# Optimization experiments

Measured on AMD Instinct MI355X. Metric: run time of the kernel, lower is better.

Reference implementation:

```python
import jax, jax.numpy as jnp
import numpy as np

N_NODES = 100000
N_EDGES = 1600000
D_IN = 64
D_OUT = 64


def setup_inputs() -> dict:
    key = jax.random.key(0)
    k1, k2, k3, k4, k5, k6 = jax.random.split(key, 6)
    x = jax.random.normal(k1, (N_NODES, D_IN), dtype=jnp.float32)
    edge_index = jax.random.randint(k2, (2, N_EDGES), 0, N_NODES, dtype=jnp.int64)
    edge_weight = jax.random.uniform(k3, (N_EDGES,), dtype=jnp.float32)
    scale = 1.0 / np.sqrt(D_IN)
    W0 = jax.random.normal(k4, (D_IN, D_OUT), dtype=jnp.float32) * scale
    W1 = jax.random.normal(k5, (D_IN, D_OUT), dtype=jnp.float32) * scale
    b = jax.random.normal(k6, (D_OUT,), dtype=jnp.float32) * 0.01
    return {"x": x, "edge_index": edge_index, "edge_weight": edge_weight,
            "W0": W0, "W1": W1, "b": b}


def reference(x, edge_index, edge_weight, W0, W1, b):
    # ChebConv K=2 with default lambda_max=2.0, sym normalization:
    # L_hat = 2L/lambda_max - I = -D^{-1/2} A D^{-1/2}
    N = x.shape[0]
    row, col = edge_index[0], edge_index[1]
    deg = jax.ops.segment_sum(edge_weight, row, num_segments=N)  # [N]
    deg_safe = jnp.where(deg > 0, deg, 1.0)
    dinv = jnp.where(deg > 0, jax.lax.rsqrt(deg_safe), 0.0)
    norm = -dinv[row] * edge_weight * dinv[col]  # [E], L_hat edge weights
    # Tx_1[i] = sum_{e: col_e = i} norm_e * x[row_e]
    Tx1 = jax.ops.segment_sum(norm[:, None] * x[row], col, num_segments=N)
    # out = lin0(Tx_0) + lin1(Tx_1) + bias
    return x @ W0 + Tx1 @ W1 + b
```

## Files before the change

### kernel.cpp

```cpp
#include <hip/hip_runtime.h>

#define N_NODES 100000
#define N_EDGES 1600000
#define D 64
#define NB 256
#define EPB (N_EDGES / NB)
#define NBUCK 3125
#define CAP 1024
#define ST 68

__global__ __launch_bounds__(256) void count_kernel(const int* __restrict__ row,
                                                    const int* __restrict__ col,
                                                    int* __restrict__ matC,
                                                    int* __restrict__ matR) {
    __shared__ int cC[NBUCK];
    __shared__ int cR[NBUCK];
    int t = threadIdx.x;
    for (int j = t; j < NBUCK; j += 256) { cC[j] = 0; cR[j] = 0; }
    __syncthreads();
    int base = blockIdx.x * EPB;
    for (int i = t; i < EPB; i += 256) {
        int e = base + i;
        atomicAdd(&cC[col[e] >> 5], 1);
        atomicAdd(&cR[row[e] >> 5], 1);
    }
    __syncthreads();
    int* mc = matC + (size_t)blockIdx.x * NBUCK;
    int* mr = matR + (size_t)blockIdx.x * NBUCK;
    for (int j = t; j < NBUCK; j += 256) { mc[j] = cC[j]; mr[j] = cR[j]; }
}

__global__ __launch_bounds__(NB) void blockscan_kernel(int* __restrict__ matC,
                                                       int* __restrict__ matR,
                                                       int* __restrict__ totalsC,
                                                       int* __restrict__ totalsR) {
    int which  = blockIdx.x / NBUCK;
    int bucket = blockIdx.x % NBUCK;
    int* mat    = which ? matR : matC;
    int* totals = which ? totalsR : totalsC;
    __shared__ int lds[NB];
    int t = threadIdx.x;
    int v = mat[(size_t)t * NBUCK + bucket];
    lds[t] = v;
    __syncthreads();
    for (int off = 1; off < NB; off <<= 1) {
        int u = (t >= off) ? lds[t - off] : 0;
        __syncthreads();
        lds[t] += u;
        __syncthreads();
    }
    mat[(size_t)t * NBUCK + bucket] = (t > 0) ? lds[t - 1] : 0;
    if (t == NB - 1) totals[bucket] = lds[NB - 1];
}

__global__ __launch_bounds__(256) void totscan_kernel(const int* __restrict__ totalsC,
                                                      int* __restrict__ bstartC,
                                                      const int* __restrict__ totalsR,
                                                      int* __restrict__ bstartR) {
    const int* tot = blockIdx.x ? totalsR : totalsC;
    int* bst       = blockIdx.x ? bstartR : bstartC;
    const int CH = (NBUCK + 255) / 256;
    __shared__ int lds[256];
    int t = threadIdx.x;
    int local[CH];
    int s = 0;
    for (int i = 0; i < CH; ++i) {
        int idx = t * CH + i;
        local[i] = (idx < NBUCK) ? tot[idx] : 0;
        s += local[i];
    }
    lds[t] = s;
    __syncthreads();
    for (int off = 1; off < 256; off <<= 1) {
        int u = (t >= off) ? lds[t - off] : 0;
        __syncthreads();
        lds[t] += u;
        __syncthreads();
    }
    int excl = (t > 0) ? lds[t - 1] : 0;
    for (int i = 0; i < CH; ++i) {
        int idx = t * CH + i;
        if (idx < NBUCK) bst[idx] = excl;
        excl += local[i];
    }
}

__global__ __launch_bounds__(256) void scatter_kernel(const int* __restrict__ row,
                                                      const int* __restrict__ col,
                                                      const float* __restrict__ w,
                                                      const int* __restrict__ matC,
                                                      const int* __restrict__ matR,
                                                      const int* __restrict__ bstartC,
                                                      const int* __restrict__ bstartR,
                                                      int2* __restrict__ crecs,
                                                      unsigned* __restrict__ rrecs) {
    __shared__ int cursC[NBUCK];
    __shared__ int cursR[NBUCK];
    int t = threadIdx.x;
    const int* offC = matC + (size_t)blockIdx.x * NBUCK;
    const int* offR = matR + (size_t)blockIdx.x * NBUCK;
    for (int j = t; j < NBUCK; j += 256) {
        cursC[j] = bstartC[j] + offC[j];
        cursR[j] = bstartR[j] + offR[j];
    }
    __syncthreads();
    int base = blockIdx.x * EPB;
    for (int i = t; i < EPB; i += 256) {
        int e = base + i;
        int r = row[e];
        int c = col[e];
        float we = w[e];
        int pC = atomicAdd(&cursC[c >> 5], 1);
        crecs[pC] = make_int2(r | ((c & 31) << 17), __float_as_int(we));
        int pR = atomicAdd(&cursR[r >> 5], 1);
        rrecs[pR] = (__float_as_uint(we) & ~31u) | (unsigned)(r & 31);
    }
}

__global__ __launch_bounds__(256) void deg_kernel(const unsigned* __restrict__ rrecs,
                                                  const int* __restrict__ bstartR,
                                                  const int* __restrict__ totalsR,
                                                  float* __restrict__ dinv) {
    __shared__ float acc[32];
    int t = threadIdx.x;
    int b = blockIdx.x;
    if (t < 32) acc[t] = 0.f;
    __syncthreads();
    int base = bstartR[b];
    int cnt  = totalsR[b];
    for (int i = t; i < cnt; i += 256) {
        unsigned v = rrecs[base + i];
        atomicAdd(&acc[v & 31u], __uint_as_float(v & ~31u));
    }
    __syncthreads();
    if (t < 32) {
        float d = acc[t];
        dinv[b * 32 + t] = d > 0.f ? rsqrtf(d) : 0.f;
    }
}

__global__ __launch_bounds__(256) void gather_out_kernel(
        const int2* __restrict__ crecs, const int* __restrict__ bstartC,
        const int* __restrict__ totalsC, const float* __restrict__ dinv,
        const float* __restrict__ x,
        const float* __restrict__ W0, const float* __restrict__ W1,
        const float* __restrict__ bias, float* __restrict__ out) {
    __shared__ __align__(16) char smem[32 * ST * 4 * 2];
    int2* raw = (int2*)smem;
    int2* srt = (int2*)(smem + 8192);
    int*  cnt32   = (int*)(smem + 16384);
    int*  start32 = cnt32 + 32;
    int*  cur32   = cnt32 + 64;
    float* xs = (float*)smem;
    float* ts = (float*)(smem + 32 * ST * 4);

    int tid = threadIdx.x;
    int b   = blockIdx.x;
    int n0  = b * 32;
    int n   = tid >> 3;
    int j   = tid & 7;

    int base = bstartC[b];
    int cnt  = totalsC[b];

    float4 acc0 = make_float4(0.f, 0.f, 0.f, 0.f);
    float4 acc1 = make_float4(0.f, 0.f, 0.f, 0.f);
    const float* xj = x + (size_t)(j << 3);

    for (int cb = 0; cb < cnt; cb += CAP) {
        int m = min(CAP, cnt - cb);
        if (tid < 32) cnt32[tid] = 0;
        __syncthreads();
        for (int i = tid; i < m; i += 256) {
            int2 rec = crecs[base + cb + i];
            raw[i] = rec;
            atomicAdd(&cnt32[((unsigned)rec.x) >> 17], 1);
        }
        __syncthreads();
        if (tid == 0) {
            int s = 0;
            for (int k = 0; k < 32; ++k) {
                int v = cnt32[k]; start32[k] = s; cur32[k] = s; s += v;
            }
        }
        __syncthreads();
        for (int i = tid; i < m; i += 256) {
            int2 rec = raw[i];
            int p = atomicAdd(&cur32[((unsigned)rec.x) >> 17], 1);
            srt[p] = rec;
        }
        __syncthreads();
        int ks = start32[n];
        int ke = ks + cnt32[n];
        int k = ks;
        for (; k + 1 < ke; k += 2) {
            int2 ra = srt[k];
            int2 rb = srt[k + 1];
            int r0 = ra.x & 0x1FFFF;
            int r1 = rb.x & 0x1FFFF;
            float c0 = __int_as_float(ra.y) * dinv[r0];
            float c1 = __int_as_float(rb.y) * dinv[r1];
            const float* p0 = xj + (size_t)r0 * D;
            const float* p1 = xj + (size_t)r1 * D;
            float4 a0 = *(const float4*)p0;
            float4 a1 = *(const float4*)(p0 + 4);
            float4 b0 = *(const float4*)p1;
            float4 b1 = *(const float4*)(p1 + 4);
            acc0.x += c0 * a0.x; acc0.y += c0 * a0.y; acc0.z += c0 * a0.z; acc0.w += c0 * a0.w;
            acc1.x += c0 * a1.x; acc1.y += c0 * a1.y; acc1.z += c0 * a1.z; acc1.w += c0 * a1.w;
            acc0.x += c1 * b0.x; acc0.y += c1 * b0.y; acc0.z += c1 * b0.z; acc0.w += c1 * b0.w;
            acc1.x += c1 * b1.x; acc1.y += c1 * b1.y; acc1.z += c1 * b1.z; acc1.w += c1 * b1.w;
        }
        if (k < ke) {
            int2 ra = srt[k];
            int r0 = ra.x & 0x1FFFF;
            float c0 = __int_as_float(ra.y) * dinv[r0];
            const float* p0 = xj + (size_t)r0 * D;
            float4 a0 = *(const float4*)p0;
            float4 a1 = *(const float4*)(p0 + 4);
            acc0.x += c0 * a0.x; acc0.y += c0 * a0.y; acc0.z += c0 * a0.z; acc0.w += c0 * a0.w;
            acc1.x += c0 * a1.x; acc1.y += c0 * a1.y; acc1.z += c0 * a1.z; acc1.w += c0 * a1.w;
        }
        __syncthreads();
    }

    float dn = -dinv[n0 + n];
    float* tp = ts + n * ST + (j << 3);
    *(float4*)tp       = make_float4(dn * acc0.x, dn * acc0.y, dn * acc0.z, dn * acc0.w);
    *(float4*)(tp + 4) = make_float4(dn * acc1.x, dn * acc1.y, dn * acc1.z, dn * acc1.w);
    for (int i = tid; i < 512; i += 256) {
        int nn = i >> 4;
        int kk = (i & 15) << 2;
        *(float4*)&xs[nn * ST + kk] = *(const float4*)(x + (size_t)n0 * D + i * 4);
    }
    __syncthreads();

    int jl = j << 3;
    float4 o0 = *(const float4*)(bias + jl);
    float4 o1 = *(const float4*)(bias + jl + 4);
    for (int k = 0; k < D; k += 4) {
        float4 av = *(const float4*)&xs[n * ST + k];
        float4 tv = *(const float4*)&ts[n * ST + k];
        #pragma unroll
        for (int u = 0; u < 4; ++u) {
            float a = (u == 0) ? av.x : (u == 1) ? av.y : (u == 2) ? av.z : av.w;
            float t = (u == 0) ? tv.x : (u == 1) ? tv.y : (u == 2) ? tv.z : tv.w;
            const float4 w00 = *(const float4*)(W0 + (size_t)(k + u) * D + jl);
            const float4 w01 = *(const float4*)(W0 + (size_t)(k + u) * D + jl + 4);
            const float4 w10 = *(const float4*)(W1 + (size_t)(k + u) * D + jl);
            const float4 w11 = *(const float4*)(W1 + (size_t)(k + u) * D + jl + 4);
            o0.x += a * w00.x + t * w10.x;
            o0.y += a * w00.y + t * w10.y;
            o0.z += a * w00.z + t * w10.z;
            o0.w += a * w00.w + t * w10.w;
            o1.x += a * w01.x + t * w11.x;
            o1.y += a * w01.y + t * w11.y;
            o1.z += a * w01.z + t * w11.z;
            o1.w += a * w01.w + t * w11.w;
        }
    }
    float* op = out + (size_t)(n0 + n) * D + jl;
    *(float4*)op       = o0;
    *(float4*)(op + 4) = o1;
}

extern "C" void kernel_launch(void* const* d_in, const int* in_sizes, int n_in,
                              void* d_out, int out_size, void* d_ws, size_t ws_size,
                              hipStream_t stream) {
    const float* x    = (const float*)d_in[0];
    const int*   eidx = (const int*)d_in[1];
    const float* ew   = (const float*)d_in[2];
    const float* W0   = (const float*)d_in[3];
    const float* W1   = (const float*)d_in[4];
    const float* b    = (const float*)d_in[5];
    float* out = (float*)d_out;

    const int* row = eidx;
    const int* col = eidx + N_EDGES;

    int2*     crecs   = (int2*)d_ws;
    unsigned* rrecs   = (unsigned*)((int*)d_ws + 2 * (size_t)N_EDGES);
    int*      matC    = (int*)rrecs + N_EDGES;
    int*      matR    = matC + (size_t)NB * NBUCK;
    int*      totalsC = matR + (size_t)NB * NBUCK;
    int*      bstartC = totalsC + NBUCK;
    int*      totalsR = bstartC + NBUCK;
    int*      bstartR = totalsR + NBUCK;
    float*    dinv    = (float*)(bstartR + NBUCK);

    count_kernel     <<<NB, 256, 0, stream>>>(row, col, matC, matR);
    blockscan_kernel <<<2 * NBUCK, NB, 0, stream>>>(matC, matR, totalsC, totalsR);
    totscan_kernel   <<<2, 256, 0, stream>>>(totalsC, bstartC, totalsR, bstartR);
    scatter_kernel   <<<NB, 256, 0, stream>>>(row, col, ew, matC, matR,
                                              bstartC, bstartR, crecs, rrecs);
    deg_kernel       <<<NBUCK, 256, 0, stream>>>(rrecs, bstartR, totalsR, dinv);
    gather_out_kernel<<<NBUCK, 256, 0, stream>>>(crecs, bstartC, totalsC, dinv,
                                                 x, W0, W1, b, out);
}
```

Baseline: 337.0 us.

## Tile the bucket-offset scan, halve partition blocks, and unroll the gather loop

```diff
diff --git a/kernel.cpp b/kernel.cpp
--- a/kernel.cpp
+++ b/kernel.cpp
@@ -3,54 +3,91 @@
 #define N_NODES 100000
 #define N_EDGES 1600000
 #define D 64
-#define NB 256
+#define NB 128
 #define EPB (N_EDGES / NB)
 #define NBUCK 3125
+#define NBUCK_PAD 3136
+#define NGRP 98
 #define CAP 1024
 #define ST 68
 
-__global__ __launch_bounds__(256) void count_kernel(const int* __restrict__ row,
+__global__ __launch_bounds__(512) void count_kernel(const int* __restrict__ row,
                                                     const int* __restrict__ col,
                                                     int* __restrict__ matC,
                                                     int* __restrict__ matR) {
-    __shared__ int cC[NBUCK];
-    __shared__ int cR[NBUCK];
-    int t = threadIdx.x;
-    for (int j = t; j < NBUCK; j += 256) { cC[j] = 0; cR[j] = 0; }
+    __shared__ int cC[NBUCK_PAD];
+    __shared__ int cR[NBUCK_PAD];
+    int t = threadIdx.x;
+    for (int j = t; j < NBUCK_PAD; j += 512) { cC[j] = 0; cR[j] = 0; }
     __syncthreads();
     int base = blockIdx.x * EPB;
-    for (int i = t; i < EPB; i += 256) {
+    for (int i = t; i < EPB; i += 512) {
         int e = base + i;
         atomicAdd(&cC[col[e] >> 5], 1);
         atomicAdd(&cR[row[e] >> 5], 1);
     }
     __syncthreads();
-    int* mc = matC + (size_t)blockIdx.x * NBUCK;
-    int* mr = matR + (size_t)blockIdx.x * NBUCK;
-    for (int j = t; j < NBUCK; j += 256) { mc[j] = cC[j]; mr[j] = cR[j]; }
-}
-
-__global__ __launch_bounds__(NB) void blockscan_kernel(int* __restrict__ matC,
-                                                       int* __restrict__ matR,
-                                                       int* __restrict__ totalsC,
-                                                       int* __restrict__ totalsR) {
-    int which  = blockIdx.x / NBUCK;
-    int bucket = blockIdx.x % NBUCK;
+    int* mc = matC + (size_t)blockIdx.x * NBUCK_PAD;
+    int* mr = matR + (size_t)blockIdx.x * NBUCK_PAD;
+    for (int j = t; j < NBUCK_PAD; j += 512) { mc[j] = cC[j]; mr[j] = cR[j]; }
+}
+
+__global__ __launch_bounds__(256) void blockscan_kernel(int* __restrict__ matC,
+                                                        int* __restrict__ matR,
+                                                        int* __restrict__ totalsC,
+                                                        int* __restrict__ totalsR) {
+    int which = blockIdx.x / NGRP;
+    int grp   = blockIdx.x % NGRP;
     int* mat    = which ? matR : matC;
     int* totals = which ? totalsR : totalsC;
-    __shared__ int lds[NB];
-    int t = threadIdx.x;
-    int v = mat[(size_t)t * NBUCK + bucket];
-    lds[t] = v;
-    __syncthreads();
-    for (int off = 1; off < NB; off <<= 1) {
-        int u = (t >= off) ? lds[t - off] : 0;
-        __syncthreads();
-        lds[t] += u;
-        __syncthreads();
-    }
-    mat[(size_t)t * NBUCK + bucket] = (t > 0) ? lds[t - 1] : 0;
-    if (t == NB - 1) totals[bucket] = lds[NB - 1];
+    int j0 = grp * 32;
+    __shared__ int tile[NB][33];
+    int t = threadIdx.x;
+    int r = t >> 1;
+    int h = t & 1;
+    {
+        const int* src = mat + (size_t)r * NBUCK_PAD + j0 + h * 16;
+        int4 v0 = *(const int4*)(src + 0);
+        int4 v1 = *(const int4*)(src + 4);
+        int4 v2 = *(const int4*)(src + 8);
+        int4 v3 = *(const int4*)(src + 12);
+        int cb = h * 16;
+        tile[r][cb+0]=v0.x;  tile[r][cb+1]=v0.y;  tile[r][cb+2]=v0.z;  tile[r][cb+3]=v0.w;
+        tile[r][cb+4]=v1.x;  tile[r][cb+5]=v1.y;  tile[r][cb+6]=v1.z;  tile[r][cb+7]=v1.w;
+        tile[r][cb+8]=v2.x;  tile[r][cb+9]=v2.y;  tile[r][cb+10]=v2.z; tile[r][cb+11]=v2.w;
+        tile[r][cb+12]=v3.x; tile[r][cb+13]=v3.y; tile[r][cb+14]=v3.z; tile[r][cb+15]=v3.w;
+    }
+    __syncthreads();
+    int g = t >> 3;
+    int l = t & 7;
+    int rows0 = l * 16;
+    int vals[16];
+    int s = 0;
+    #pragma unroll
+    for (int i = 0; i < 16; ++i) { vals[i] = tile[rows0 + i][g]; s += vals[i]; }
+    int inc = s;
+    #pragma unroll
+    for (int d = 1; d < 8; d <<= 1) {
+        int u = __shfl_up(inc, d, 8);
+        if (l >= d) inc += u;
+    }
+    int excl = inc - s;
+    #pragma unroll
+    for (int i = 0; i < 16; ++i) { int e2 = excl; excl += vals[i]; tile[rows0 + i][g] = e2; }
+    if (l == 7) totals[j0 + g] = inc;
+    __syncthreads();
+    {
+        int* dst = mat + (size_t)r * NBUCK_PAD + j0 + h * 16;
+        int cb = h * 16;
+        int4 v0 = make_int4(tile[r][cb+0],  tile[r][cb+1],  tile[r][cb+2],  tile[r][cb+3]);
+        int4 v1 = make_int4(tile[r][cb+4],  tile[r][cb+5],  tile[r][cb+6],  tile[r][cb+7]);
+        int4 v2 = make_int4(tile[r][cb+8],  tile[r][cb+9],  tile[r][cb+10], tile[r][cb+11]);
+        int4 v3 = make_int4(tile[r][cb+12], tile[r][cb+13], tile[r][cb+14], tile[r][cb+15]);
+        *(int4*)(dst + 0)  = v0;
+        *(int4*)(dst + 4)  = v1;
+        *(int4*)(dst + 8)  = v2;
+        *(int4*)(dst + 12) = v3;
+    }
 }
 
 __global__ __launch_bounds__(256) void totscan_kernel(const int* __restrict__ totalsC,
@@ -59,14 +96,14 @@
                                                       int* __restrict__ bstartR) {
     const int* tot = blockIdx.x ? totalsR : totalsC;
     int* bst       = blockIdx.x ? bstartR : bstartC;
-    const int CH = (NBUCK + 255) / 256;
+    const int CH = (NBUCK_PAD + 255) / 256;
     __shared__ int lds[256];
     int t = threadIdx.x;
     int local[CH];
     int s = 0;
     for (int i = 0; i < CH; ++i) {
         int idx = t * CH + i;
-        local[i] = (idx < NBUCK) ? tot[idx] : 0;
+        local[i] = (idx < NBUCK_PAD) ? tot[idx] : 0;
         s += local[i];
     }
     lds[t] = s;
@@ -80,12 +117,12 @@
     int excl = (t > 0) ? lds[t - 1] : 0;
     for (int i = 0; i < CH; ++i) {
         int idx = t * CH + i;
-        if (idx < NBUCK) bst[idx] = excl;
+        if (idx < NBUCK_PAD) bst[idx] = excl;
         excl += local[i];
     }
 }
 
-__global__ __launch_bounds__(256) void scatter_kernel(const int* __restrict__ row,
+__global__ __launch_bounds__(512) void scatter_kernel(const int* __restrict__ row,
                                                       const int* __restrict__ col,
                                                       const float* __restrict__ w,
                                                       const int* __restrict__ matC,
@@ -97,15 +134,15 @@
     __shared__ int cursC[NBUCK];
     __shared__ int cursR[NBUCK];
     int t = threadIdx.x;
-    const int* offC = matC + (size_t)blockIdx.x * NBUCK;
-    const int* offR = matR + (size_t)blockIdx.x * NBUCK;
-    for (int j = t; j < NBUCK; j += 256) {
+    const int* offC = matC + (size_t)blockIdx.x * NBUCK_PAD;
+    const int* offR = matR + (size_t)blockIdx.x * NBUCK_PAD;
+    for (int j = t; j < NBUCK; j += 512) {
         cursC[j] = bstartC[j] + offC[j];
         cursR[j] = bstartR[j] + offR[j];
     }
     __syncthreads();
     int base = blockIdx.x * EPB;
-    for (int i = t; i < EPB; i += 256) {
+    for (int i = t; i < EPB; i += 512) {
         int e = base + i;
         int r = row[e];
         int c = col[e];
@@ -138,6 +175,10 @@
         dinv[b * 32 + t] = d > 0.f ? rsqrtf(d) : 0.f;
     }
 }
+
+#define FMA8(cc, av, bv)                                                       \
+    acc0.x += cc * av.x; acc0.y += cc * av.y; acc0.z += cc * av.z; acc0.w += cc * av.w; \
+    acc1.x += cc * bv.x; acc1.y += cc * bv.y; acc1.z += cc * bv.z; acc1.w += cc * bv.w;
 
 __global__ __launch_bounds__(256) void gather_out_kernel(
         const int2* __restrict__ crecs, const int* __restrict__ bstartC,
@@ -173,15 +214,22 @@
         __syncthreads();
         for (int i = tid; i < m; i += 256) {
             int2 rec = crecs[base + cb + i];
+            int r = rec.x & 0x1FFFF;
+            rec.y = __float_as_int(__int_as_float(rec.y) * dinv[r]);
             raw[i] = rec;
             atomicAdd(&cnt32[((unsigned)rec.x) >> 17], 1);
         }
         __syncthreads();
-        if (tid == 0) {
-            int s = 0;
-            for (int k = 0; k < 32; ++k) {
-                int v = cnt32[k]; start32[k] = s; cur32[k] = s; s += v;
+        if (tid < 32) {
+            int v = cnt32[tid];
+            int inc = v;
+            #pragma unroll
+            for (int d = 1; d < 32; d <<= 1) {
+                int u = __shfl_up(inc, d, 32);
+                if (tid >= d) inc += u;
             }
+            start32[tid] = inc - v;
+            cur32[tid]   = inc - v;
         }
         __syncthreads();
         for (int i = tid; i < m; i += 256) {
@@ -193,33 +241,34 @@
         int ks = start32[n];
         int ke = ks + cnt32[n];
         int k = ks;
-        for (; k + 1 < ke; k += 2) {
-            int2 ra = srt[k];
-            int2 rb = srt[k + 1];
-            int r0 = ra.x & 0x1FFFF;
-            int r1 = rb.x & 0x1FFFF;
-            float c0 = __int_as_float(ra.y) * dinv[r0];
-            float c1 = __int_as_float(rb.y) * dinv[r1];
-            const float* p0 = xj + (size_t)r0 * D;
-            const float* p1 = xj + (size_t)r1 * D;
-            float4 a0 = *(const float4*)p0;
-            float4 a1 = *(const float4*)(p0 + 4);
-            float4 b0 = *(const float4*)p1;
-            float4 b1 = *(const float4*)(p1 + 4);
-            acc0.x += c0 * a0.x; acc0.y += c0 * a0.y; acc0.z += c0 * a0.z; acc0.w += c0 * a0.w;
-            acc1.x += c0 * a1.x; acc1.y += c0 * a1.y; acc1.z += c0 * a1.z; acc1.w += c0 * a1.w;
-            acc0.x += c1 * b0.x; acc0.y += c1 * b0.y; acc0.z += c1 * b0.z; acc0.w += c1 * b0.w;
-            acc1.x += c1 * b1.x; acc1.y += c1 * b1.y; acc1.z += c1 * b1.z; acc1.w += c1 * b1.w;
-        }
-        if (k < ke) {
-            int2 ra = srt[k];
-            int r0 = ra.x & 0x1FFFF;
-            float c0 = __int_as_float(ra.y) * dinv[r0];
-            const float* p0 = xj + (size_t)r0 * D;
-            float4 a0 = *(const float4*)p0;
-            float4 a1 = *(const float4*)(p0 + 4);
-            acc0.x += c0 * a0.x; acc0.y += c0 * a0.y; acc0.z += c0 * a0.z; acc0.w += c0 * a0.w;
-            acc1.x += c0 * a1.x; acc1.y += c0 * a1.y; acc1.z += c0 * a1.z; acc1.w += c0 * a1.w;
+        for (; k + 3 < ke; k += 4) {
+            int2 e0 = srt[k + 0];
+            int2 e1 = srt[k + 1];
+            int2 e2 = srt[k + 2];
+            int2 e3 = srt[k + 3];
+            const float* p0 = xj + (size_t)(e0.x & 0x1FFFF) * D;
+            const float* p1 = xj + (size_t)(e1.x & 0x1FFFF) * D;
+            const float* p2 = xj + (size_t)(e2.x & 0x1FFFF) * D;
+            const float* p3 = xj + (size_t)(e3.x & 0x1FFFF) * D;
+            float c0 = __int_as_float(e0.y);
+            float c1 = __int_as_float(e1.y);
+            float c2 = __int_as_float(e2.y);
+            float c3 = __int_as_float(e3.y);
+            float4 a0 = *(const float4*)p0, b0 = *(const float4*)(p0 + 4);
+            float4 a1 = *(const float4*)p1, b1 = *(const float4*)(p1 + 4);
+            float4 a2 = *(const float4*)p2, b2 = *(const float4*)(p2 + 4);
+            float4 a3 = *(const float4*)p3, b3 = *(const float4*)(p3 + 4);
+            FMA8(c0, a0, b0)
+            FMA8(c1, a1, b1)
+            FMA8(c2, a2, b2)
+            FMA8(c3, a3, b3)
+        }
+        for (; k < ke; ++k) {
+            int2 e0 = srt[k];
+            const float* p0 = xj + (size_t)(e0.x & 0x1FFFF) * D;
+            float c0 = __int_as_float(e0.y);
+            float4 a0 = *(const float4*)p0, b0 = *(const float4*)(p0 + 4);
+            FMA8(c0, a0, b0)
         }
         __syncthreads();
     }
@@ -281,17 +330,17 @@
     int2*     crecs   = (int2*)d_ws;
     unsigned* rrecs   = (unsigned*)((int*)d_ws + 2 * (size_t)N_EDGES);
     int*      matC    = (int*)rrecs + N_EDGES;
-    int*      matR    = matC + (size_t)NB * NBUCK;
-    int*      totalsC = matR + (size_t)NB * NBUCK;
-    int*      bstartC = totalsC + NBUCK;
-    int*      totalsR = bstartC + NBUCK;
-    int*      bstartR = totalsR + NBUCK;
-    float*    dinv    = (float*)(bstartR + NBUCK);
-
-    count_kernel     <<<NB, 256, 0, stream>>>(row, col, matC, matR);
-    blockscan_kernel <<<2 * NBUCK, NB, 0, stream>>>(matC, matR, totalsC, totalsR);
+    int*      matR    = matC + (size_t)NB * NBUCK_PAD;
+    int*      totalsC = matR + (size_t)NB * NBUCK_PAD;
+    int*      bstartC = totalsC + NBUCK_PAD;
+    int*      totalsR = bstartC + NBUCK_PAD;
+    int*      bstartR = totalsR + NBUCK_PAD;
+    float*    dinv    = (float*)(bstartR + NBUCK_PAD);
+
+    count_kernel     <<<NB, 512, 0, stream>>>(row, col, matC, matR);
+    blockscan_kernel <<<2 * NGRP, 256, 0, stream>>>(matC, matR, totalsC, totalsR);
     totscan_kernel   <<<2, 256, 0, stream>>>(totalsC, bstartC, totalsR, bstartR);
-    scatter_kernel   <<<NB, 256, 0, stream>>>(row, col, ew, matC, matR,
+    scatter_kernel   <<<NB, 512, 0, stream>>>(row, col, ew, matC, matR,
                                               bstartC, bstartR, crecs, rrecs);
     deg_kernel       <<<NBUCK, 256, 0, stream>>>(rrecs, bstartR, totalsR, dinv);
     gather_out_kernel<<<NBUCK, 256, 0, stream>>>(crecs, bstartC, totalsC, dinv,
```

Result: faster. 292.5 us (-13.2%).
